# Kernel tuning notes

Hardware: AMD Instinct MI355X
Metric: run time of the kernel (lower is better)

## Reference

```python
import jax, jax.numpy as jnp
from jax import lax
import numpy as np

B, L, D_MODEL = 2, 1024, 1024
D_STATE, D_CONV, EXPAND = 16, 4, 2
D_INNER = EXPAND * D_MODEL
DT_RANK = (D_MODEL + 15) // 16


def setup_inputs() -> dict:
    key = jax.random.key(0)
    ks = jax.random.split(key, 12)
    s = 0.02
    inp = {
        "x": jax.random.normal(ks[0], (B, L, D_MODEL), jnp.float32),
        "in_w": jax.random.normal(ks[1], (2, D_MODEL, 2 * D_INNER), jnp.float32) * s,
        "conv_w": jax.random.normal(ks[2], (2, D_INNER, D_CONV), jnp.float32) * 0.2,
        "conv_b": jax.random.normal(ks[3], (2, D_INNER), jnp.float32) * 0.02,
        "xp_w": jax.random.normal(ks[4], (2, D_INNER, DT_RANK + 2 * D_STATE), jnp.float32) * s,
        "dt_w": jax.random.normal(ks[5], (2, DT_RANK, D_INNER), jnp.float32) * (DT_RANK ** -0.5),
        # inverse-softplus of dt in [1e-3, 0.1], standard Mamba dt init
        "dt_b": jnp.log(jnp.expm1(jax.random.uniform(ks[6], (2, D_INNER), jnp.float32, 1e-3, 0.1))),
        # S4D-real init: A = -[1..d_state]
        "A_log": jnp.broadcast_to(jnp.log(jnp.arange(1, D_STATE + 1, dtype=jnp.float32)), (2, D_INNER, D_STATE)),
        "D": jnp.ones((2, D_INNER), jnp.float32),
        "out_w": jax.random.normal(ks[7], (2, D_INNER, D_MODEL), jnp.float32) * s,
        "proj_w": jax.random.normal(ks[8], (2 * D_MODEL, D_MODEL), jnp.float32) * s,
        "proj_b": jnp.zeros((D_MODEL,), jnp.float32),
    }
    return inp


def _mamba(x, in_w, conv_w, conv_b, xp_w, dt_w, dt_b, A_log, Dskip, out_w):
    b, l, _ = x.shape
    d_inner = conv_w.shape[0]
    d_conv = conv_w.shape[1]
    dt_rank = dt_w.shape[0]
    d_state = A_log.shape[-1]

    xz = x @ in_w                              # (b, l, 2*d_inner)
    xi, z = jnp.split(xz, 2, axis=-1)

    # causal depthwise conv1d
    xp = jnp.pad(xi, ((0, 0), (d_conv - 1, 0), (0, 0)))
    xc = lax.conv_general_dilated(
        xp.transpose(0, 2, 1), conv_w[:, None, :],
        window_strides=(1,), padding="VALID",
        dimension_numbers=("NCH", "OIH", "NCH"),
        feature_group_count=d_inner)
    xc = jax.nn.silu(xc.transpose(0, 2, 1) + conv_b)   # (b, l, d_inner)

    dbc = xc @ xp_w
    dt, Bm, Cm = jnp.split(dbc, [dt_rank, dt_rank + d_state], axis=-1)
    dt = jax.nn.softplus(dt @ dt_w + dt_b)             # (b, l, d_inner)
    A = -jnp.exp(A_log)                                # (d_inner, d_state)

    def step(h, inp):
        dt_t, B_t, C_t, x_t = inp                      # (b,d), (b,n), (b,n), (b,d)
        dA = jnp.exp(dt_t[..., None] * A)              # (b, d, n)
        h = h * dA + (dt_t * x_t)[..., None] * B_t[:, None, :]
        y = jnp.einsum("bdn,bn->bd", h, C_t)
        return h, y

    h0 = jnp.zeros((b, d_inner, d_state), x.dtype)
    xs = (dt.transpose(1, 0, 2), Bm.transpose(1, 0, 2),
          Cm.transpose(1, 0, 2), xc.transpose(1, 0, 2))
    _, ys = lax.scan(step, h0, xs)                     # (l, b, d_inner)
    y = ys.transpose(1, 0, 2) + xc * Dskip
    y = y * jax.nn.silu(z)
    return y @ out_w


def reference(x, in_w, conv_w, conv_b, xp_w, dt_w, dt_b, A_log, D, out_w, proj_w, proj_b):
    y_fwd = _mamba(x, in_w[0], conv_w[0], conv_b[0], xp_w[0], dt_w[0], dt_b[0], A_log[0], D[0], out_w[0])
    xr = x[:, ::-1, :]
    y_bwd = _mamba(xr, in_w[1], conv_w[1], conv_b[1], xp_w[1], dt_w[1], dt_b[1], A_log[1], D[1], out_w[1])[:, ::-1, :]
    cat = jnp.concatenate([y_fwd, y_bwd], axis=-1)
    return cat @ proj_w + proj_b
```

## Files before the change

### kernel.cpp

```cpp
#include <hip/hip_runtime.h>
#include <hip/hip_bf16.h>

#define B_    2
#define LSEQ  1024
#define DM    1024
#define DI    2048
#define DTR   64
#define DS    16
#define MROWS 2048
#define NCH   32
#define CL    32
#define KSPL  16

typedef __bf16 bf16x8 __attribute__((ext_vector_type(8)));
typedef short  s16x8  __attribute__((ext_vector_type(8)));
typedef float  f32x4  __attribute__((ext_vector_type(4)));

typedef __attribute__((address_space(1))) const unsigned int g_u32;
typedef __attribute__((address_space(3))) unsigned int l_u32;

__device__ __forceinline__ unsigned short f2bf(float f) {
  unsigned int u = __builtin_bit_cast(unsigned int, f);
  u += 0x7fffu + ((u >> 16) & 1u);
  return (unsigned short)(u >> 16);
}
__device__ __forceinline__ float b2f(unsigned short u) {
  unsigned int x = ((unsigned int)u) << 16;
  return __builtin_bit_cast(float, x);
}

__device__ __forceinline__ void gload16(void* lds, const void* g) {
  __builtin_amdgcn_global_load_lds((g_u32*)g, (l_u32*)lds, 16, 0, 0);
}

__device__ __forceinline__ f32x4 mfma_bf16_16x16x32(s16x8 a, s16x8 b, f32x4 c) {
  return __builtin_amdgcn_mfma_f32_16x16x32_bf16(
      __builtin_bit_cast(bf16x8, a), __builtin_bit_cast(bf16x8, b), c, 0, 0, 0);
}

__device__ __forceinline__ float softplus_f(float x) {
  return fmaxf(x, 0.f) + log1pf(__expf(-fabsf(x)));
}

template<int EPI, int BN>
__global__ __launch_bounds__(256)
void bgemm(const unsigned short* __restrict__ A, long sAd, int lda, int revA,
           const unsigned short* __restrict__ Bt, long sBtd,
           const float* __restrict__ bias, int sBiasD,
           void* __restrict__ C, long sCd, int ldc, int revC, int colOffDir,
           int K)
{
  constexpr int NI = BN / 32;
  const int dir = blockIdx.z;
  A  += (long)dir * sAd;
  Bt += (long)dir * sBtd;
  const float* bp = bias ? (bias + (long)dir * sBiasD) : nullptr;

  const int m0 = blockIdx.y * 128;
  const int n0 = blockIdx.x * BN;

  __shared__ __align__(16) unsigned short sA[2][128 * 32];
  __shared__ __align__(16) unsigned short sB[2][BN * 32];

  const int t    = threadIdx.x;
  const int wave = t >> 6;
  const int lane = t & 63;
  const int l15  = lane & 15;
  const int l4   = lane >> 4;
  const int wr   = wave >> 1;
  const int wc   = wave & 1;

  auto STAGE = [&](unsigned short* dA, unsigned short* dB, int k0) {
    #pragma unroll
    for (int i = 0; i < 2; i++) {
      const int ch  = (wave * 2 + i) * 64 + lane;
      const int row = ch >> 2;
      const int kcol = (ch & 3) ^ ((row >> 1) & 3);
      const int mm = m0 + row;
      const int mr = (revA && dir) ? ((mm & ~(LSEQ - 1)) | (LSEQ - 1 - (mm & (LSEQ - 1)))) : mm;
      gload16(dA + (long)ch * 8, A + (long)mr * lda + k0 + kcol * 8);
    }
    #pragma unroll
    for (int i = 0; i < BN / 64; i++) {
      const int ch  = (wave * (BN / 64) + i) * 64 + lane;
      const int row = ch >> 2;
      const int kcol = (ch & 3) ^ ((row >> 1) & 3);
      gload16(dB + (long)ch * 8, Bt + (long)(n0 + row) * K + k0 + kcol * 8);
    }
  };

  f32x4 acc[4][NI];
  #pragma unroll
  for (int i = 0; i < 4; i++)
    #pragma unroll
    for (int j = 0; j < NI; j++)
      acc[i][j] = f32x4{0.f, 0.f, 0.f, 0.f};

  STAGE(sA[0], sB[0], 0);
  __syncthreads();

  const int nt = K >> 5;
  for (int ti = 0; ti < nt; ++ti) {
    const int cur = ti & 1;
    if (ti + 1 < nt) STAGE(sA[cur ^ 1], sB[cur ^ 1], (ti + 1) << 5);

    s16x8 af[4], bf[NI];
    #pragma unroll
    for (int mi = 0; mi < 4; mi++) {
      const int r = wr * 64 + mi * 16 + l15;
      af[mi] = *(const s16x8*)(sA[cur] + (r * 32 + ((l4 ^ ((r >> 1) & 3)) << 3)));
    }
    #pragma unroll
    for (int ni = 0; ni < NI; ni++) {
      const int r = wc * (BN / 2) + ni * 16 + l15;
      bf[ni] = *(const s16x8*)(sB[cur] + (r * 32 + ((l4 ^ ((r >> 1) & 3)) << 3)));
    }
    #pragma unroll
    for (int mi = 0; mi < 4; mi++)
      #pragma unroll
      for (int ni = 0; ni < NI; ni++)
        acc[mi][ni] = mfma_bf16_16x16x32(af[mi], bf[ni], acc[mi][ni]);
    __syncthreads();
  }

  const int colOff = dir * colOffDir;
  float*          Cf = (float*)C + (long)dir * sCd;
  unsigned short* Cb = (unsigned short*)C + (long)dir * sCd;
  #pragma unroll
  for (int mi = 0; mi < 4; mi++) {
    #pragma unroll
    for (int r = 0; r < 4; r++) {
      const int mm = m0 + wr * 64 + mi * 16 + (l4 << 2) + r;
      const int mr = (revC && dir) ? ((mm & ~(LSEQ - 1)) | (LSEQ - 1 - (mm & (LSEQ - 1)))) : mm;
      #pragma unroll
      for (int ni = 0; ni < NI; ni++) {
        const int col = n0 + wc * (BN / 2) + ni * 16 + l15;
        float v = acc[mi][ni][r];
        if (EPI == 1) v += bp[col];
        if (EPI == 3) v = softplus_f(v + bp[col]);
        if (EPI == 2) Cb[(long)mr * ldc + colOff + col] = f2bf(v);
        else          Cf[(long)mr * ldc + colOff + col] = v;
      }
    }
  }
}

__global__ __launch_bounds__(256)
void bgemm96(const unsigned short* __restrict__ A,
             const unsigned short* __restrict__ Bt,
             float* __restrict__ dbc4)
{
  const int ks  = blockIdx.x;
  const int m0  = blockIdx.y * 128;
  const int dir = blockIdx.z;
  const int kbase = ks * (2048 / KSPL);

  const unsigned short* Ad  = A  + (long)dir * MROWS * DI;
  const unsigned short* Btd = Bt + (long)dir * 96 * DI;

  __shared__ __align__(16) unsigned short sA[128 * 32];
  __shared__ __align__(16) unsigned short sB[96 * 32];

  const int t    = threadIdx.x;
  const int wave = t >> 6;
  const int lane = t & 63;
  const int l15  = lane & 15;
  const int l4   = lane >> 4;
  const int wr   = wave >> 1;
  const int wc   = wave & 1;

  f32x4 acc[4][3];
  #pragma unroll
  for (int i = 0; i < 4; i++)
    #pragma unroll
    for (int j = 0; j < 3; j++)
      acc[i][j] = f32x4{0.f, 0.f, 0.f, 0.f};

  for (int k0 = 0; k0 < 2048 / KSPL; k0 += 32) {
    #pragma unroll
    for (int i = 0; i < 2; i++) {
      const int ch  = (wave * 2 + i) * 64 + lane;
      const int row = ch >> 2;
      const int kcol = (ch & 3) ^ ((row >> 1) & 3);
      gload16(sA + (long)ch * 8, Ad + (long)(m0 + row) * DI + kbase + k0 + kcol * 8);
    }
    {
      const int ch  = wave * 64 + lane;
      const int row = ch >> 2;
      const int kcol = (ch & 3) ^ ((row >> 1) & 3);
      gload16(sB + (long)ch * 8, Btd + (long)row * DI + kbase + k0 + kcol * 8);
    }
    if (wave < 2) {
      const int ch  = 256 + wave * 64 + lane;
      const int row = ch >> 2;
      const int kcol = (ch & 3) ^ ((row >> 1) & 3);
      gload16(sB + (long)ch * 8, Btd + (long)row * DI + kbase + k0 + kcol * 8);
    }
    __syncthreads();

    s16x8 af[4], bf[3];
    #pragma unroll
    for (int mi = 0; mi < 4; mi++) {
      const int r = wr * 64 + mi * 16 + l15;
      af[mi] = *(const s16x8*)(sA + (r * 32 + ((l4 ^ ((r >> 1) & 3)) << 3)));
    }
    #pragma unroll
    for (int ni = 0; ni < 3; ni++) {
      const int r = wc * 48 + ni * 16 + l15;
      bf[ni] = *(const s16x8*)(sB + (r * 32 + ((l4 ^ ((r >> 1) & 3)) << 3)));
    }
    #pragma unroll
    for (int mi = 0; mi < 4; mi++)
      #pragma unroll
      for (int ni = 0; ni < 3; ni++)
        acc[mi][ni] = mfma_bf16_16x16x32(af[mi], bf[ni], acc[mi][ni]);
    __syncthreads();
  }

  float* outp = dbc4 + (long)ks * 4096 * 96;
  #pragma unroll
  for (int mi = 0; mi < 4; mi++) {
    #pragma unroll
    for (int r = 0; r < 4; r++) {
      const long grow = (long)dir * MROWS + m0 + wr * 64 + mi * 16 + (l4 << 2) + r;
      #pragma unroll
      for (int ni = 0; ni < 3; ni++) {
        const int col = wc * 48 + ni * 16 + l15;
        outp[grow * 96 + col] = acc[mi][ni][r];
      }
    }
  }
}

__global__ __launch_bounds__(256)
void reduce_k(const float* __restrict__ dbc4, float* __restrict__ dbc,
              unsigned short* __restrict__ dbcb)
{
  const long i = ((long)blockIdx.x * 256 + threadIdx.x) << 2;
  f32x4 s = *(const f32x4*)(dbc4 + i);
  #pragma unroll
  for (int ks = 1; ks < KSPL; ks++) {
    f32x4 v = *(const f32x4*)(dbc4 + (long)ks * 4096 * 96 + i);
    s.x += v.x; s.y += v.y; s.z += v.z; s.w += v.w;
  }
  *(f32x4*)(dbc + i) = s;
  ushort4 ob;
  ob.x = f2bf(s.x); ob.y = f2bf(s.y); ob.z = f2bf(s.z); ob.w = f2bf(s.w);
  *(ushort4*)(dbcb + i) = ob;
}

__global__ __launch_bounds__(256)
void convert_bf16_k(const float* __restrict__ src, unsigned short* __restrict__ dst)
{
  const long i = ((long)blockIdx.x * 256 + threadIdx.x) << 2;
  const float4 v = *(const float4*)(src + i);
  ushort4 o;
  o.x = f2bf(v.x); o.y = f2bf(v.y); o.z = f2bf(v.z); o.w = f2bf(v.w);
  *(ushort4*)(dst + i) = o;
}

__global__ __launch_bounds__(256)
void transpose_bf16_k(const float* __restrict__ src, long sSd, int R, int C,
                      unsigned short* __restrict__ dst, long sDd)
{
  const int dir = blockIdx.z;
  src += (long)dir * sSd;
  dst += (long)dir * sDd;
  const int c0 = blockIdx.x * 32;
  const int r0 = blockIdx.y * 32;
  __shared__ float tile[32][33];
  const int t = threadIdx.x;
  const int lr = t >> 3, lc = (t & 7) << 2;
  const float4 v = *(const float4*)(src + (long)(r0 + lr) * C + c0 + lc);
  tile[lr][lc + 0] = v.x; tile[lr][lc + 1] = v.y;
  tile[lr][lc + 2] = v.z; tile[lr][lc + 3] = v.w;
  __syncthreads();
  const int oc = t >> 3, orr = (t & 7) << 2;
  ushort4 o;
  o.x = f2bf(tile[orr + 0][oc]);
  o.y = f2bf(tile[orr + 1][oc]);
  o.z = f2bf(tile[orr + 2][oc]);
  o.w = f2bf(tile[orr + 3][oc]);
  *(ushort4*)(dst + (long)(c0 + oc) * R + r0 + orr) = o;
}

__global__ __launch_bounds__(256)
void conv_silu_k(const unsigned short* __restrict__ xzb,
                 unsigned short* __restrict__ xcb,
                 const float* __restrict__ cw, const float* __restrict__ cb)
{
  const long idx = (long)blockIdx.x * blockDim.x + threadIdx.x;
  const int d4  = (int)(idx & 511);
  const int m   = (int)((idx >> 9) & 2047);
  const int dir = (int)(idx >> 20);
  const int l = m & (LSEQ - 1);
  const int d = d4 << 2;

  const unsigned short* xip = xzb + ((long)dir * MROWS + m) * 4096 + d;
  const float* w = cw + ((long)dir * DI + d) * 4;

  float4 wv0 = *(const float4*)(w + 0);
  float4 wv1 = *(const float4*)(w + 4);
  float4 wv2 = *(const float4*)(w + 8);
  float4 wv3 = *(const float4*)(w + 12);

  float4 acc = *(const float4*)(cb + (long)dir * DI + d);

  #pragma unroll
  for (int j = 0; j < 4; j++) {
    const int lj = l - 3 + j;
    if (lj >= 0) {
      const ushort4 xv = *(const ushort4*)(xip + (long)(j - 3) * 4096);
      acc.x += b2f(xv.x) * ((const float*)&wv0)[j];
      acc.y += b2f(xv.y) * ((const float*)&wv1)[j];
      acc.z += b2f(xv.z) * ((const float*)&wv2)[j];
      acc.w += b2f(xv.w) * ((const float*)&wv3)[j];
    }
  }

  float4 o;
  o.x = acc.x / (1.f + __expf(-acc.x));
  o.y = acc.y / (1.f + __expf(-acc.y));
  o.z = acc.z / (1.f + __expf(-acc.z));
  o.w = acc.w / (1.f + __expf(-acc.w));
  ushort4 ob;
  ob.x = f2bf(o.x); ob.y = f2bf(o.y); ob.z = f2bf(o.z); ob.w = f2bf(o.w);
  *(ushort4*)(xcb + ((long)dir * MROWS + m) * DI + d) = ob;
}

__global__ __launch_bounds__(256)
void scan_p1(const float* __restrict__ dt, const float* __restrict__ dbc,
             const unsigned short* __restrict__ xcb, const float* __restrict__ A_log,
             float* __restrict__ Pbuf, float* __restrict__ Ebuf)
{
  const int blk  = blockIdx.x;
  const int c    = blk & (NCH - 1);
  const int dblk = (blk >> 5) & 7;
  const int b    = (blk >> 8) & 1;
  const int dir  = blk >> 9;
  const int d    = (dblk << 8) + threadIdx.x;

  const long row0 = (long)dir * MROWS + (long)b * LSEQ + (long)c * CL;
  const float* dtp = dt + row0 * DI + d;
  const unsigned short* xcp = xcb + row0 * DI + d;
  const float* bc  = dbc + row0 * 96;

  float Av[DS];
  #pragma unroll
  for (int n = 0; n < DS; n++)
    Av[n] = -__expf(A_log[((long)dir * DI + d) * DS + n]);

  __shared__ float sB[CL][DS];
  #pragma unroll
  for (int i = 0; i < 2; i++) {
    const int e = threadIdx.x * 2 + i;
    sB[e >> 4][e & 15] = bc[(long)(e >> 4) * 96 + 64 + (e & 15)];
  }
  __syncthreads();

  float h[DS];
  #pragma unroll
  for (int n = 0; n < DS; n++) h[n] = 0.f;
  float sdt = 0.f;

  for (int li = 0; li < CL; li++) {
    const float dtv = dtp[(long)li * DI];
    const float xv  = b2f(xcp[(long)li * DI]);
    const float u = dtv * xv;
    sdt += dtv;
    #pragma unroll
    for (int n = 0; n < DS; n++)
      h[n] = h[n] * __expf(dtv * Av[n]) + u * sB[li][n];
  }

  const long slot = ((long)((dir * 2 + b) * NCH + c)) * DS;
  #pragma unroll
  for (int n = 0; n < DS; n++) Ebuf[(slot + n) * DI + d] = h[n];
  #pragma unroll
  for (int n = 0; n < DS; n++) Pbuf[(slot + n) * DI + d] = __expf(Av[n] * sdt);
}

__global__ __launch_bounds__(256)
void scan_p2(float* __restrict__ Pbuf, const float* __restrict__ Ebuf)
{
  const int blk  = blockIdx.x;
  const int dblk = blk & 7;
  const int b    = (blk >> 3) & 1;
  const int dir  = blk >> 4;
  const int d    = (dblk << 8) + threadIdx.x;

  float h[DS];
  #pragma unroll
  for (int n = 0; n < DS; n++) h[n] = 0.f;

  for (int c = 0; c < NCH; c++) {
    const long slot = ((long)((dir * 2 + b) * NCH + c)) * DS;
    float p[DS], e[DS];
    #pragma unroll
    for (int n = 0; n < DS; n++) p[n] = Pbuf[(slot + n) * DI + d];
    #pragma unroll
    for (int n = 0; n < DS; n++) e[n] = Ebuf[(slot + n) * DI + d];
    #pragma unroll
    for (int n = 0; n < DS; n++) Pbuf[(slot + n) * DI + d] = h[n];
    #pragma unroll
    for (int n = 0; n < DS; n++) h[n] = p[n] * h[n] + e[n];
  }
}

__global__ __launch_bounds__(256)
void scan_p3(const float* __restrict__ dt, const float* __restrict__ dbc,
             const unsigned short* __restrict__ xcb, const unsigned short* __restrict__ xzb,
             const float* __restrict__ A_log, const float* __restrict__ Dp,
             const float* __restrict__ Hbuf, unsigned short* __restrict__ ymul)
{
  const int blk  = blockIdx.x;
  const int c    = blk & (NCH - 1);
  const int dblk = (blk >> 5) & 7;
  const int b    = (blk >> 8) & 1;
  const int dir  = blk >> 9;
  const int d    = (dblk << 8) + threadIdx.x;

  const long row0 = (long)dir * MROWS + (long)b * LSEQ + (long)c * CL;
  const float* dtp = dt + row0 * DI + d;
  const unsigned short* xcp = xcb + row0 * DI + d;
  const unsigned short* zp  = xzb + row0 * 4096 + DI + d;
  unsigned short* ymp = ymul + row0 * DI + d;
  const float* bc  = dbc + row0 * 96;

  float Av[DS];
  #pragma unroll
  for (int n = 0; n < DS; n++)
    Av[n] = -__expf(A_log[((long)dir * DI + d) * DS + n]);
  const float Dd = Dp[(long)dir * DI + d];

  const long slot = ((long)((dir * 2 + b) * NCH + c)) * DS;
  float h[DS];
  #pragma unroll
  for (int n = 0; n < DS; n++) h[n] = Hbuf[(slot + n) * DI + d];

  __shared__ float sBC[CL][32];
  #pragma unroll
  for (int i = 0; i < 4; i++) {
    const int e = threadIdx.x * 4 + i;
    sBC[e >> 5][e & 31] = bc[(long)(e >> 5) * 96 + 64 + (e & 31)];
  }
  __syncthreads();

  for (int li = 0; li < CL; li++) {
    const float dtv = dtp[(long)li * DI];
    const float xv  = b2f(xcp[(long)li * DI]);
    const float zv  = b2f(zp[(long)li * 4096]);
    const float u = dtv * xv;
    float y = 0.f;
    #pragma unroll
    for (int n = 0; n < DS; n++) {
      const float dA = __expf(dtv * Av[n]);
      h[n] = h[n] * dA + u * sBC[li][n];
      y += h[n] * sBC[li][16 + n];
    }
    const float sig = 1.f / (1.f + __expf(-zv));
    ymp[(long)li * DI] = f2bf((y + xv * Dd) * (zv * sig));
  }
}

extern "C" void kernel_launch(void* const* d_in, const int* in_sizes, int n_in,
                              void* d_out, int out_size, void* d_ws, size_t ws_size,
                              hipStream_t stream)
{
  const float* x      = (const float*)d_in[0];
  const float* in_w   = (const float*)d_in[1];
  const float* conv_w = (const float*)d_in[2];
  const float* conv_b = (const float*)d_in[3];
  const float* xp_w   = (const float*)d_in[4];
  const float* dt_w   = (const float*)d_in[5];
  const float* dt_b   = (const float*)d_in[6];
  const float* A_log  = (const float*)d_in[7];
  const float* Dp     = (const float*)d_in[8];
  const float* out_w  = (const float*)d_in[9];
  const float* proj_w = (const float*)d_in[10];
  const float* proj_b = (const float*)d_in[11];
  float* out = (float*)d_out;

  const long M1 = 1024 * 1024;
  float* ws    = (float*)d_ws;
  unsigned short* xzb = (unsigned short*)ws;
  unsigned short* xcb = (unsigned short*)(ws + 8 * M1);
  float* dbc   = ws + 12 * M1;
  float* slotD = dbc + 393216;
  float* regR  = slotD + 8 * M1;
  unsigned short* xb    = (unsigned short*)regR;
  unsigned short* in_wt = (unsigned short*)(regR + M1);
  float*          dbc4  = regR;
  unsigned short* dbcb  = (unsigned short*)(regR + 6 * M1);
  unsigned short* xpwt  = (unsigned short*)(regR + 6 * M1 + 262144);
  unsigned short* dtwt  = (unsigned short*)(regR + 6 * M1 + 524288);
  float* Pbuf = regR;
  float* Ebuf = regR + 4 * M1;
  unsigned short* ymulb = (unsigned short*)(regR + 4 * M1);
  float*          dt   = slotD;
  unsigned short* owt  = (unsigned short*)slotD;
  unsigned short* pwt  = (unsigned short*)(slotD + 2 * M1);
  unsigned short* catb = (unsigned short*)xzb;

  hipLaunchKernelGGL(transpose_bf16_k, dim3(3, 64, 2), dim3(256), 0, stream,
                     xp_w, (long)DI * 96, DI, 96, xpwt, (long)96 * DI);
  hipLaunchKernelGGL(transpose_bf16_k, dim3(64, 2, 2), dim3(256), 0, stream,
                     dt_w, (long)DTR * DI, DTR, DI, dtwt, (long)DI * DTR);
  hipLaunchKernelGGL(convert_bf16_k, dim3(2048), dim3(256), 0, stream, x, xb);
  hipLaunchKernelGGL(transpose_bf16_k, dim3(128, 32, 2), dim3(256), 0, stream,
                     in_w, (long)1024 * 4096, 1024, 4096, in_wt, (long)4096 * 1024);

  hipLaunchKernelGGL(HIP_KERNEL_NAME(bgemm<2, 128>), dim3(32, 16, 2), dim3(256), 0, stream,
                     xb, (long)0, 1024, 1,
                     in_wt, (long)4096 * 1024,
                     (const float*)nullptr, 0,
                     xzb, (long)MROWS * 4096, 4096, 0, 0,
                     1024);

  hipLaunchKernelGGL(conv_silu_k, dim3(8192), dim3(256), 0, stream,
                     xzb, xcb, conv_w, conv_b);

  hipLaunchKernelGGL(bgemm96, dim3(KSPL, 16, 2), dim3(256), 0, stream,
                     xcb, xpwt, dbc4);
  hipLaunchKernelGGL(reduce_k, dim3(384), dim3(256), 0, stream, dbc4, dbc, dbcb);

  hipLaunchKernelGGL(HIP_KERNEL_NAME(bgemm<3, 128>), dim3(16, 16, 2), dim3(256), 0, stream,
                     dbcb, (long)MROWS * 96, 96, 0,
                     dtwt, (long)DI * DTR,
                     dt_b, DI,
                     dt, (long)MROWS * DI, DI, 0, 0,
                     DTR);

  hipLaunchKernelGGL(scan_p1, dim3(1024), dim3(256), 0, stream,
                     dt, dbc, xcb, A_log, Pbuf, Ebuf);
  hipLaunchKernelGGL(scan_p2, dim3(32), dim3(256), 0, stream,
                     Pbuf, Ebuf);
  hipLaunchKernelGGL(scan_p3, dim3(1024), dim3(256), 0, stream,
                     dt, dbc, xcb, xzb, A_log, Dp, Pbuf, ymulb);

  hipLaunchKernelGGL(transpose_bf16_k, dim3(32, 64, 2), dim3(256), 0, stream,
                     out_w, (long)2048 * 1024, 2048, 1024, owt, (long)1024 * 2048);
  hipLaunchKernelGGL(transpose_bf16_k, dim3(32, 64, 1), dim3(256), 0, stream,
                     proj_w, (long)0, 2048, 1024, pwt, (long)0);

  hipLaunchKernelGGL(HIP_KERNEL_NAME(bgemm<2, 64>), dim3(16, 16, 2), dim3(256), 0, stream,
                     ymulb, (long)MROWS * DI, DI, 0,
                     owt, (long)1024 * 2048,
                     (const float*)nullptr, 0,
                     catb, (long)0, 2048, 1, 1024,
                     2048);

  hipLaunchKernelGGL(HIP_KERNEL_NAME(bgemm<1, 64>), dim3(16, 16, 1), dim3(256), 0, stream,
                     catb, (long)0, 2048, 0,
                     pwt, (long)0,
                     proj_b, 0,
                     out, (long)0, 1024, 0, 0,
                     2048);
}
```

Baseline: 314.4 us.

## Use 256x256-tile 512-thread GEMM for input projection

Replaces the 128x128-tile generic GEMM for the in_proj (x @ in_w) with a dedicated 256x256-tile kernel using 8 waves, double-buffered LDS staging through global_load_lds with XOR swizzling, and a block-index remap for L2 locality. Larger tiles raise arithmetic intensity and cut global and L2 traffic per FLOP, and the explicit waitcnt pipelining lets loads overlap MFMA work. In exchange it uses 128KB of LDS per block with only 256 blocks in the grid, which reduces occupancy and wave-level parallelism across the CUs.

```diff
diff --git a/kernel.cpp b/kernel.cpp
--- a/kernel.cpp
+++ b/kernel.cpp
@@ -40,6 +40,125 @@
 
 __device__ __forceinline__ float softplus_f(float x) {
   return fmaxf(x, 0.f) + log1pf(__expf(-fabsf(x)));
+}
+
+__global__ __launch_bounds__(512, 2)
+void bgemm256(const unsigned short* __restrict__ A, long sAd, int lda, int revA,
+              const unsigned short* __restrict__ Bt, long sBtd,
+              unsigned short* __restrict__ C, long sCd, int ldc,
+              int K)
+{
+  const int dir = blockIdx.z;
+  A  += (long)dir * sAd;
+  Bt += (long)dir * sBtd;
+  C  += (long)dir * sCd;
+
+  const int bid2 = blockIdx.y * 16 + blockIdx.x;
+  const int logical = (bid2 & 7) * 16 + (bid2 >> 3);
+  const int m0 = (logical & 7) * 256;
+  const int n0 = (logical >> 3) * 256;
+
+  __shared__ __align__(16) unsigned short sL[2][2][16384];
+
+  const int tid  = threadIdx.x;
+  const int wave = tid >> 6;
+  const int lane = tid & 63;
+  const int l15  = lane & 15;
+  const int l4   = lane >> 4;
+  const int wr   = wave >> 2;
+  const int wc   = wave & 3;
+
+  auto STAGE = [&](int buf, int kt) {
+    const int kb = kt * 64;
+    #pragma unroll
+    for (int i = 0; i < 8; i++) {
+      const int ch  = i * 512 + tid;
+      const int mat = ch >> 11;
+      const int lch = ch & 2047;
+      const int row = lch >> 3;
+      const int ku  = (lch & 7) ^ (row & 7);
+      const void* src;
+      if (mat == 0) {
+        const int mm = m0 + row;
+        const int mr = (revA && dir) ? ((mm & ~(LSEQ - 1)) | (LSEQ - 1 - (mm & (LSEQ - 1)))) : mm;
+        src = A + (long)mr * lda + kb + ku * 8;
+      } else {
+        src = Bt + (long)(n0 + row) * K + kb + ku * 8;
+      }
+      gload16(&sL[buf][mat][lch * 8], src);
+    }
+  };
+
+  f32x4 acc[8][4];
+  #pragma unroll
+  for (int i = 0; i < 8; i++)
+    #pragma unroll
+    for (int j = 0; j < 4; j++)
+      acc[i][j] = f32x4{0.f, 0.f, 0.f, 0.f};
+
+  const int T = K >> 6;
+  STAGE(0, 0);
+  STAGE(1, 1);
+
+  for (int t = 0; t < T; ++t) {
+    const int buf = t & 1;
+    if (t + 1 < T) { asm volatile("s_waitcnt vmcnt(8)" ::: "memory"); }
+    else           { asm volatile("s_waitcnt vmcnt(0)" ::: "memory"); }
+    __builtin_amdgcn_sched_barrier(0);
+    __builtin_amdgcn_s_barrier();
+    __builtin_amdgcn_sched_barrier(0);
+
+    const unsigned short* sa = sL[buf][0];
+    const unsigned short* sb = sL[buf][1];
+
+    #pragma unroll
+    for (int q = 0; q < 4; q++) {
+      const int qm = q >> 1, qn = q & 1;
+      s16x8 af[4][2], bf_[2][2];
+      #pragma unroll
+      for (int mi = 0; mi < 4; mi++) {
+        const int R = wr * 128 + qm * 64 + mi * 16 + l15;
+        #pragma unroll
+        for (int ks = 0; ks < 2; ks++)
+          af[mi][ks] = *(const s16x8*)(sa + R * 64 + (((ks * 4 + l4) ^ (R & 7)) << 3));
+      }
+      #pragma unroll
+      for (int ni = 0; ni < 2; ni++) {
+        const int Cc = wc * 64 + qn * 32 + ni * 16 + l15;
+        #pragma unroll
+        for (int ks = 0; ks < 2; ks++)
+          bf_[ni][ks] = *(const s16x8*)(sb + Cc * 64 + (((ks * 4 + l4) ^ (Cc & 7)) << 3));
+      }
+      __builtin_amdgcn_s_setprio(1);
+      #pragma unroll
+      for (int mi = 0; mi < 4; mi++)
+        #pragma unroll
+        for (int ni = 0; ni < 2; ni++)
+          #pragma unroll
+          for (int ks = 0; ks < 2; ks++)
+            acc[qm * 4 + mi][qn * 2 + ni] =
+                mfma_bf16_16x16x32(af[mi][ks], bf_[ni][ks], acc[qm * 4 + mi][qn * 2 + ni]);
+      __builtin_amdgcn_s_setprio(0);
+    }
+
+    __builtin_amdgcn_sched_barrier(0);
+    __builtin_amdgcn_s_barrier();
+    __builtin_amdgcn_sched_barrier(0);
+    if (t + 2 < T) STAGE(buf, t + 2);
+  }
+
+  #pragma unroll
+  for (int mi = 0; mi < 8; mi++) {
+    #pragma unroll
+    for (int r = 0; r < 4; r++) {
+      const int mr = m0 + wr * 128 + mi * 16 + (l4 << 2) + r;
+      #pragma unroll
+      for (int ni = 0; ni < 4; ni++) {
+        const int col = n0 + wc * 64 + ni * 16 + l15;
+        C[(long)mr * ldc + col] = f2bf(acc[mi][ni][r]);
+      }
+    }
+  }
 }
 
 template<int EPI, int BN>
@@ -510,11 +629,10 @@
   hipLaunchKernelGGL(transpose_bf16_k, dim3(128, 32, 2), dim3(256), 0, stream,
                      in_w, (long)1024 * 4096, 1024, 4096, in_wt, (long)4096 * 1024);
 
-  hipLaunchKernelGGL(HIP_KERNEL_NAME(bgemm<2, 128>), dim3(32, 16, 2), dim3(256), 0, stream,
+  hipLaunchKernelGGL(bgemm256, dim3(16, 8, 2), dim3(512), 0, stream,
                      xb, (long)0, 1024, 1,
                      in_wt, (long)4096 * 1024,
-                     (const float*)nullptr, 0,
-                     xzb, (long)MROWS * 4096, 4096, 0, 0,
+                     xzb, (long)MROWS * 4096, 4096,
                      1024);
 
   hipLaunchKernelGGL(conv_silu_k, dim3(8192), dim3(256), 0, stream,
```

After: 306.9 us. -2.4%, faster.
